# Optimization experiments

Measured on AMD Instinct MI355X. Metric: run time of the kernel, lower is better.

Reference implementation:

```python
import jax, jax.numpy as jnp
import numpy as np

# --- problem constants (match init_kwargs / input_specs) ---
FS = 50.0            # sampling rate (Hz)
WINDOW_FREQ = 0.5    # running-abs-mean window (Hz); >0 -> RAM whitening branch
F1, F2 = 0.1, 10.0   # taper corner frequencies (Hz)
NCH, NPTS = 1000, 30000
XCOR = 2 * NPTS - 1          # 59999
FAST = 65536                 # nextpow2(XCOR)


def setup_inputs() -> dict:
    key = jax.random.key(0)
    k1, k2 = jax.random.split(key)
    return {
        "data1": jax.random.normal(k1, (NCH, NPTS), dtype=jnp.float32),
        "data2": jax.random.normal(k2, (NCH, NPTS), dtype=jnp.float32),
    }


def _running_abs_mean_whiten(rfft, nwin):
    """Vectorized equivalent of per-channel running_absolute_mean:
    pad |spec| by nwin edge values each side, box-filter (scipy 'same'
    alignment => window tmp[i+off+1 : i+off+1+nwin], off=(nwin-1)//2),
    then divide spectrum by the smoothed magnitude."""
    nch, nf = rfft.shape
    off = (nwin - 1) // 2
    a = jnp.abs(rfft)  # [nch, nf]
    tmp = jnp.concatenate(
        [jnp.broadcast_to(a[:, :1], (nch, nwin)), a,
         jnp.broadcast_to(a[:, -1:], (nch, nwin))], axis=1)  # [nch, nf+2*nwin]
    cs = jnp.pad(jnp.cumsum(tmp, axis=1), ((0, 0), (1, 0)))   # leading zero
    smoothed = (cs[:, off + 1 + nwin: off + 1 + nwin + nf]
                - cs[:, off + 1: off + 1 + nf]) / nwin
    return jnp.nan_to_num(rfft / smoothed)


def _spectral_whitening(rfft, df):
    nf = rfft.shape[-1]
    idxf1 = int(np.floor(F1 / df))
    idxf2 = int(np.ceil(F2 / df))
    nwin = int(WINDOW_FREQ / df)
    w = _running_abs_mean_whiten(rfft, nwin)
    # cosine-squared tapers outside [f1, f2]
    taper_lo = jnp.cos(jnp.linspace(np.pi / 2, np.pi, idxf1)) ** 2
    taper_hi = jnp.cos(jnp.linspace(np.pi, np.pi / 2, nf - idxf2)) ** 2
    w = w.at[:, :idxf1].multiply(taper_lo)
    w = w.at[:, idxf2:].multiply(taper_hi)
    return w


def reference(data1, data2):
    df = FS / FAST
    f1 = jnp.fft.rfft(data1, n=FAST, axis=-1)
    f2 = jnp.fft.rfft(data2, n=FAST, axis=-1)
    f1 = _spectral_whitening(f1, df)
    f2 = _spectral_whitening(f2, df)
    cc = jnp.fft.irfft(jnp.conj(f1) * f2, n=FAST, axis=-1)  # [nch, FAST]
    cc = jnp.roll(cc, FAST // 2, axis=-1)
    start = FAST // 2 - XCOR // 2
    return cc[:, start:start + XCOR]  # [nch, 2*npts-1]
```

## Files before the change

### kernel.cpp

```cpp
#include <hip/hip_runtime.h>

#define PI_F 3.14159265358979323846f

#define NCH   1000
#define NPTS  30000
#define NHALF 15000
#define NFFT  32768
#define NBF32 1024
#define STR   32770
#define XCOR  59999

#define UC 0.99518472667219693f
#define US 0.09801714032956060f

__device__ __forceinline__ float2 cadd(float2 a, float2 b){ return make_float2(a.x+b.x, a.y+b.y); }
__device__ __forceinline__ float2 csub(float2 a, float2 b){ return make_float2(a.x-b.x, a.y-b.y); }
__device__ __forceinline__ float2 cmul(float2 a, float2 b){ return make_float2(a.x*b.x - a.y*b.y, a.x*b.y + a.y*b.x); }
__device__ __forceinline__ float2 conjmul(float2 a, float2 b){
  return make_float2(a.x*b.x + a.y*b.y, a.x*b.y - a.y*b.x);
}

template<int S>
__device__ __forceinline__ float2 mulIs(float2 z){ return make_float2(-(float)S*z.y, (float)S*z.x); }

template<int S>
__device__ __forceinline__ void dft8(float2 v[8]){
  const float r2 = 0.7071067811865476f;
  const float sf = (float)S;
  float2 ea=cadd(v[0],v[4]), eb=csub(v[0],v[4]);
  float2 ec=cadd(v[2],v[6]), ed=csub(v[2],v[6]);
  float2 oa=cadd(v[1],v[5]), ob=csub(v[1],v[5]);
  float2 oc=cadd(v[3],v[7]), od=csub(v[3],v[7]);
  float2 ied=mulIs<S>(ed), iod=mulIs<S>(od);
  float2 E0=cadd(ea,ec), E2=csub(ea,ec), E1=cadd(eb,ied), E3=csub(eb,ied);
  float2 O0=cadd(oa,oc), O2=csub(oa,oc), O1=cadd(ob,iod), O3=csub(ob,iod);
  float2 T1 = make_float2(r2*(O1.x - sf*O1.y), r2*(O1.y + sf*O1.x));
  float2 T2 = mulIs<S>(O2);
  float2 T3 = make_float2(r2*(-O3.x - sf*O3.y), r2*(sf*O3.x - O3.y));
  v[0]=cadd(E0,O0); v[4]=csub(E0,O0);
  v[1]=cadd(E1,T1); v[5]=csub(E1,T1);
  v[2]=cadd(E2,T2); v[6]=csub(E2,T2);
  v[3]=cadd(E3,T3); v[7]=csub(E3,T3);
}

template<int S>
__device__ __forceinline__ void dft4(float2 v[4]){
  float2 t0=cadd(v[0],v[2]), t1=csub(v[0],v[2]);
  float2 t2=cadd(v[1],v[3]), t3=mulIs<S>(csub(v[1],v[3]));
  v[0]=cadd(t0,t2); v[2]=csub(t0,t2);
  v[1]=cadd(t1,t3); v[3]=csub(t1,t3);
}

template<int S>
__device__ __forceinline__ void dft32(float2 v[32]){
  constexpr float TC[22] = {
    1.f, 0.98078528040323044f, 0.92387953251128674f, 0.83146961230254524f,
    0.70710678118654757f, 0.55557023301960218f, 0.38268343236508978f, 0.19509032201612825f,
    0.f, -0.19509032201612825f, -0.38268343236508978f, -0.55557023301960218f,
    -0.70710678118654757f, -0.83146961230254524f, -0.92387953251128674f, -0.98078528040323044f,
    -1.f, -0.98078528040323044f, -0.92387953251128674f, -0.83146961230254524f,
    -0.70710678118654757f, -0.55557023301960218f };
  constexpr float TS[22] = {
    0.f, 0.19509032201612825f, 0.38268343236508978f, 0.55557023301960218f,
    0.70710678118654757f, 0.83146961230254524f, 0.92387953251128674f, 0.98078528040323044f,
    1.f, 0.98078528040323044f, 0.92387953251128674f, 0.83146961230254524f,
    0.70710678118654757f, 0.55557023301960218f, 0.38268343236508978f, 0.19509032201612825f,
    0.f, -0.19509032201612825f, -0.38268343236508978f, -0.55557023301960218f,
    -0.70710678118654757f, -0.83146961230254524f };
  float2 y[4][8];
  #pragma unroll
  for (int b = 0; b < 4; ++b)
    #pragma unroll
    for (int a = 0; a < 8; ++a) y[b][a] = v[4*a + b];
  #pragma unroll
  for (int b = 0; b < 4; ++b) dft8<S>(y[b]);
  #pragma unroll
  for (int b = 1; b < 4; ++b)
    #pragma unroll
    for (int k1 = 1; k1 < 8; ++k1) {
      int m = b*k1;
      float2 w = make_float2(TC[m], (float)S * TS[m]);
      y[b][k1] = cmul(y[b][k1], w);
    }
  #pragma unroll
  for (int k1 = 0; k1 < 8; ++k1) {
    float2 z[4] = { y[0][k1], y[1][k1], y[2][k1], y[3][k1] };
    dft4<S>(z);
    #pragma unroll
    for (int k2 = 0; k2 < 4; ++k2) v[k1 + 8*k2] = z[k2];
  }
}

template<int S>
__device__ __forceinline__ void stage_twiddle32(float2 v[32], float ang){
  float s1,c1,s8,c8;
  __sincosf(ang, &s1, &c1);
  __sincosf(8.f*ang, &s8, &c8);
  float2 w1 = make_float2(c1, s1), w8 = make_float2(c8, s8);
  float2 w16 = cmul(w8, w8), w24 = cmul(w16, w8);
  float2 base[4] = { make_float2(1.f, 0.f), w8, w16, w24 };
  #pragma unroll
  for (int m = 0; m < 4; ++m) {
    float2 wr = base[m];
    if (m > 0) v[8*m] = cmul(v[8*m], wr);
    #pragma unroll
    for (int l = 1; l < 8; ++l) { wr = cmul(wr, w1); v[8*m+l] = cmul(v[8*m+l], wr); }
  }
}

__global__ __launch_bounds__(256) void fft_fwd_fused(const float* __restrict__ d1, const float* __restrict__ d2,
                                                     float2* __restrict__ out, int cb, int ch0)
{
  __shared__ float2 lds[256*33];
  const int bid = blockIdx.x;
  const int c = bid >> 2, b = bid & 3;
  const int t = threadIdx.x;
  const float* src = (c < cb) ? (d1 + (size_t)(ch0 + c) * NPTS)
                              : (d2 + (size_t)(ch0 + c - cb) * NPTS);
  const float2* src2 = reinterpret_cast<const float2*>(src);

  const int j1 = 8*b + (t & 7) + 32*(t >> 3);
  float2 v[32];
  #pragma unroll
  for (int r = 0; r < 32; ++r) {
    int m = j1 + (r << 10);
    v[r] = (m < NHALF) ? src2[m] : make_float2(0.f, 0.f);
  }
  dft32<-1>(v);
  #pragma unroll
  for (int r = 0; r < 32; ++r) lds[t*33 + r] = v[r];
  __syncthreads();

  const int d = t >> 5, jm = t & 31;
  #pragma unroll
  for (int r = 0; r < 32; ++r) v[r] = lds[(d + 8*r)*33 + jm];
  stage_twiddle32<-1>(v, -(2.0f*PI_F) * (float)jm * (1.0f/1024.0f));
  dft32<-1>(v);
  const int j2 = 256*b + t;
  float2* dst = out + (size_t)c * STR + ((j2 >> 5) << 10) + jm;
  #pragma unroll
  for (int r = 0; r < 32; ++r) dst[(size_t)(r << 5)] = v[r];
}

template<int LG, int S>
__global__ __launch_bounds__(256) void fft_pass32(const float2* __restrict__ in, float2* __restrict__ out)
{
  int tid = blockIdx.x*256 + threadIdx.x;
  int c = tid >> 10;
  int j = tid & (NBF32-1);
  const float2* src = in + (size_t)c * STR;
  float2 v[32];
  #pragma unroll
  for (int r = 0; r < 32; ++r) v[r] = src[j + (r << 10)];
  constexpr int NS = 1 << LG;
  int jm = j & (NS - 1);
  if constexpr (LG > 0) {
    float ang = (float)S * (2.0f*PI_F) * (float)jm / (float)(NS*32);
    stage_twiddle32<S>(v, ang);
  }
  dft32<S>(v);
  int idxD = ((j >> LG) << (LG+5)) + jm;
  float2* dst = out + (size_t)c * STR + idxD;
  #pragma unroll
  for (int r = 0; r < 32; ++r) dst[(size_t)(r << LG)] = v[r];
}

__device__ __forceinline__ int padidx(int m){ return m + (m >> 5); }

__global__ __launch_bounds__(1024) void whiten_kernel(float2* __restrict__ buf)
{
  const int ch = blockIdx.x;
  const int t  = threadIdx.x;
  float2* Z = buf + (size_t)ch * STR;
  __shared__ float s[33793];
  __shared__ float wsums[16];

  float2 X[33];
  #pragma unroll
  for (int i = 0; i < 33; ++i) {
    int k = i*1024 + t;
    if (i < 32 || t == 0) {
      float2 zk = Z[k & (NFFT-1)];
      float2 zn = Z[(NFFT - k) & (NFFT-1)];
      float2 xe = make_float2(0.5f*(zk.x+zn.x), 0.5f*(zk.y-zn.y));
      float2 xh = make_float2(0.5f*(zk.x-zn.x), 0.5f*(zk.y+zn.y));
      float2 xo = make_float2(xh.y, -xh.x);
      float ang = -PI_F * (float)k * (1.0f/32768.0f);
      float sn, cs; __sincosf(ang, &sn, &cs);
      float2 w = make_float2(cs, sn);
      X[i] = cadd(xe, cmul(w, xo));
      s[padidx(k)] = sqrtf(X[i].x*X[i].x + X[i].y*X[i].y);
    }
  }
  __syncthreads();

  const int base = t*32;
  float sum = 0.f;
  #pragma unroll
  for (int q = 0; q < 32; ++q) sum += s[padidx(base+q)];
  if (t == 1023) sum += s[padidx(32768)];
  const int lane = t & 63, wid = t >> 6;
  float v = sum;
  #pragma unroll
  for (int off = 1; off < 64; off <<= 1) {
    float u = __shfl_up(v, off);
    if (lane >= off) v += u;
  }
  if (lane == 63) wsums[wid] = v;
  __syncthreads();
  float wexcl = 0.f;
  for (int w = 0; w < 16; ++w) wexcl += (w < wid) ? wsums[w] : 0.f;
  float run = wexcl + (v - sum);
  #pragma unroll
  for (int q = 0; q < 32; ++q) {
    int idx = padidx(base+q);
    run += s[idx];
    s[idx] = run;
  }
  if (t == 1023) { int idx = padidx(32768); run += s[idx]; s[idx] = run; }
  __syncthreads();

  const float a0 = s[padidx(0)];
  const float alast = s[padidx(32768)] - s[padidx(32767)];
  #pragma unroll
  for (int i = 0; i < 33; ++i) {
    int k = i*1024 + t;
    if (i < 32 || t == 0) {
      int hi = k + 327; if (hi > 32768) hi = 32768;
      int lom1 = k - 328;
      float Shi = s[padidx(hi)];
      float Slo = (lom1 >= 0) ? s[padidx(lom1)] : 0.f;
      float lc = (k < 327) ? (float)(327 - k) : 0.f;
      float rc = (k > 32441) ? (float)(k - 32441) : 0.f;
      float smoothed = (lc*a0 + (Shi - Slo) + rc*alast) * (1.0f/655.0f);
      float2 wv;
      if (smoothed > 0.f) {
        float inv = 1.0f / smoothed;
        wv = make_float2(X[i].x*inv, X[i].y*inv);
      } else wv = make_float2(0.f, 0.f);
      float tp = 1.0f;
      if (k < 131)        { float th = (float)k * (PI_F/260.0f);           float sn = __sinf(th); tp = sn*sn; }
      else if (k >= 13108){ float th = (float)(k-13108) * (PI_F/39320.0f); float cs = __cosf(th); tp = cs*cs; }
      wv.x *= tp; wv.y *= tp;
      Z[k] = wv;
    }
  }
}

__device__ __forceinline__ float2 pack_zinv(float2 Ck, float2 Cm, float2 pw){
  const float scale = 1.0f/32768.0f;
  float2 xe = make_float2(0.5f*(Ck.x+Cm.x), 0.5f*(Ck.y-Cm.y));
  float2 d  = make_float2(0.5f*(Ck.x-Cm.x), 0.5f*(Ck.y+Cm.y));
  float2 xo = cmul(pw, d);
  return make_float2((xe.x - xo.y)*scale, (xe.y + xo.x)*scale);
}

__global__ __launch_bounds__(256) void cross_inv0_pair(const float2* __restrict__ W,
                                                       float2* __restrict__ out0, int cb)
{
  __shared__ float2 zbs[256*33];
  const int bid = blockIdx.x;
  const int c = bid >> 1;
  const int t = threadIdx.x;
  const int p = ((bid & 1) << 8) + t;
  const float2* W1 = W + (size_t)c * STR;
  const float2* W2 = W + (size_t)(cb + c) * STR;
  const float scale = 1.0f/32768.0f;
  float2 zA[32];
  float2* zB = zbs + t*33;

  if (p != 0) {
    const int q = 1024 - p;
    float sp, cp; __sincosf(PI_F*(float)p*(1.0f/32768.0f), &sp, &cp);
    float2 pw = make_float2(cp, sp);
    const float2 pstep = make_float2(UC, US);
    #pragma unroll
    for (int r = 0; r < 32; ++r) {
      int m  = p + (r << 10);
      int mm = q + ((31 - r) << 10);
      float2 Ck = conjmul(W1[m],  W2[m]);
      float2 Cm = conjmul(W1[mm], W2[mm]);
      zA[r]    = pack_zinv(Ck, Cm, pw);
      zB[31-r] = pack_zinv(Cm, Ck, make_float2(-pw.x, pw.y));
      pw = cmul(pw, pstep);
    }
  } else {
    {
      float2 Ck = conjmul(W1[0], W2[0]);
      float2 Cm = conjmul(W1[32768], W2[32768]);
      zA[0] = pack_zinv(Ck, Cm, make_float2(1.f, 0.f));
    }
    #pragma unroll
    for (int i = 1; i < 16; ++i) {
      int k = i << 10, km = 32768 - k;
      float2 Ck = conjmul(W1[k],  W2[k]);
      float2 Cm = conjmul(W1[km], W2[km]);
      float sp2, cp2; __sincosf(PI_F*(float)k*(1.0f/32768.0f), &sp2, &cp2);
      zA[i]    = pack_zinv(Ck, Cm, make_float2(cp2, sp2));
      zA[32-i] = pack_zinv(Cm, Ck, make_float2(-cp2, sp2));
    }
    {
      float2 Ck = conjmul(W1[16384], W2[16384]);
      zA[16] = make_float2(Ck.x*scale, -Ck.y*scale);
    }
    #pragma unroll
    for (int i = 0; i < 16; ++i) {
      int k = (i << 10) + 512, km = 32768 - k;
      float2 Ck = conjmul(W1[k],  W2[k]);
      float2 Cm = conjmul(W1[km], W2[km]);
      float sp2, cp2; __sincosf(PI_F*(float)k*(1.0f/32768.0f), &sp2, &cp2);
      zB[i]    = pack_zinv(Ck, Cm, make_float2(cp2, sp2));
      zB[31-i] = pack_zinv(Cm, Ck, make_float2(-cp2, sp2));
    }
  }

  dft32<1>(zA);
  {
    float4* o4 = reinterpret_cast<float4*>(out0 + (size_t)c*STR + (size_t)p*32);
    #pragma unroll
    for (int r = 0; r < 32; r += 2)
      o4[r>>1] = make_float4(zA[r].x, zA[r].y, zA[r+1].x, zA[r+1].y);
  }
  {
    float2 zq[32];
    #pragma unroll
    for (int r = 0; r < 32; ++r) zq[r] = zB[r];
    dft32<1>(zq);
    const int jout = (p == 0) ? 512 : (1024 - p);
    float4* o4 = reinterpret_cast<float4*>(out0 + (size_t)c*STR + (size_t)jout*32);
    #pragma unroll
    for (int r = 0; r < 32; r += 2)
      o4[r>>1] = make_float4(zq[r].x, zq[r].y, zq[r+1].x, zq[r+1].y);
  }
}

__global__ __launch_bounds__(256) void fft_inv_fused2(const float2* __restrict__ in,
                                                      float* __restrict__ out, int ch0)
{
  __shared__ float2 lds[32*268];
  const int c = blockIdx.x;
  const int b = blockIdx.y;
  const int t = threadIdx.x;
  const int li = t & 7, s = t >> 3;
  const int l = 8*b + li;
  const float2* src = in + (size_t)c * STR;

  {
    const int j1 = l + 32*s;
    float2 v[32];
    #pragma unroll
    for (int r = 0; r < 32; ++r) v[r] = src[j1 + (r << 10)];
    stage_twiddle32<1>(v, (2.0f*PI_F) * (float)l * (1.0f/1024.0f));
    dft32<1>(v);
    #pragma unroll
    for (int r = 0; r < 32; ++r) lds[s*268 + li*33 + r] = v[r];
  }
  __syncthreads();

  const int q = s;
  const int j2 = l + 32*q;
  float2 v[32];
  #pragma unroll
  for (int r2 = 0; r2 < 32; ++r2) v[r2] = lds[r2*268 + li*33 + q];
  stage_twiddle32<1>(v, (2.0f*PI_F) * (float)j2 * (1.0f/32768.0f));
  dft32<1>(v);

  float* o = out + (size_t)(ch0 + c) * XCOR;
  #pragma unroll
  for (int r = 0; r < 32; ++r) {
    int n = j2 + (r << 10);
    int m = 2*n;
    int j1o = (m <= 29999) ? (m + 29999) : ((m >= 35537) ? (m - 35537) : -1);
    if (j1o >= 0) o[j1o] = v[r].x;
    int m2 = m + 1;
    int j2o = (m2 <= 29999) ? (m2 + 29999) : ((m2 >= 35537) ? (m2 - 35537) : -1);
    if (j2o >= 0) o[j2o] = v[r].y;
  }
}

__global__ void diag_kernel(float* out, float vv){ if (threadIdx.x==0 && blockIdx.x==0) out[0] = vv; }

extern "C" void kernel_launch(void* const* d_in, const int* in_sizes, int n_in,
                              void* d_out, int out_size, void* d_ws, size_t ws_size,
                              hipStream_t stream)
{
  const float* d1 = (const float*)d_in[0];
  const float* d2 = (const float*)d_in[1];
  float* out = (float*)d_out;

  const size_t bytesPerCh = 2ULL * 2ULL * (size_t)STR * sizeof(float2);
  int CB = (int)(ws_size / bytesPerCh);
  if (CB > NCH) CB = NCH;
  if (CB < 1) { diag_kernel<<<1,1,0,stream>>>(out, (float)ws_size); return; }

  float2* bufA = (float2*)d_ws;
  float2* bufB = bufA + (size_t)2 * CB * STR;

  for (int ch0 = 0; ch0 < NCH; ch0 += CB) {
    int cb = (NCH - ch0 < CB) ? (NCH - ch0) : CB;
    int nch2 = 2*cb;
    dim3 thr(256);

    fft_fwd_fused     <<<dim3(nch2*4), thr, 0, stream>>>(d1, d2, bufA, cb, ch0);
    fft_pass32<10,-1> <<<dim3(nch2*4), thr, 0, stream>>>(bufA, bufB);

    whiten_kernel     <<<dim3(nch2), dim3(1024), 0, stream>>>(bufB);

    cross_inv0_pair   <<<dim3(cb*2), thr, 0, stream>>>(bufB, bufA, cb);

    fft_inv_fused2    <<<dim3(cb, 4), thr, 0, stream>>>(bufA, out, ch0);
  }
}
```

Measured before the change: 1.298 ms.

## Split fused inverse FFT into two passes and use recurrence twiddles in whitening

The whitening kernel now computes its unpack twiddles and cosine taper values with complex-multiply recurrences instead of a sincos call per element, which cuts transcendental work. The fused two-stage inverse FFT kernel, which exchanged data through shared memory, is replaced by a separate fft_pass32 launch followed by a simpler final radix-32 kernel. That adds a global-memory round trip and an extra launch but removes the LDS transpose and its barrier. The recurrences can accumulate float rounding error over 33 steps.

```diff
diff --git a/kernel.cpp b/kernel.cpp
--- a/kernel.cpp
+++ b/kernel.cpp
@@ -176,20 +176,23 @@
   __shared__ float wsums[16];
 
   float2 X[33];
-  #pragma unroll
-  for (int i = 0; i < 33; ++i) {
-    int k = i*1024 + t;
-    if (i < 32 || t == 0) {
-      float2 zk = Z[k & (NFFT-1)];
-      float2 zn = Z[(NFFT - k) & (NFFT-1)];
-      float2 xe = make_float2(0.5f*(zk.x+zn.x), 0.5f*(zk.y-zn.y));
-      float2 xh = make_float2(0.5f*(zk.x-zn.x), 0.5f*(zk.y+zn.y));
-      float2 xo = make_float2(xh.y, -xh.x);
-      float ang = -PI_F * (float)k * (1.0f/32768.0f);
-      float sn, cs; __sincosf(ang, &sn, &cs);
-      float2 w = make_float2(cs, sn);
-      X[i] = cadd(xe, cmul(w, xo));
-      s[padidx(k)] = sqrtf(X[i].x*X[i].x + X[i].y*X[i].y);
+  {
+    float s0, c0; __sincosf(-PI_F*(float)t*(1.0f/32768.0f), &s0, &c0);
+    float2 uw = make_float2(c0, s0);
+    const float2 uwstep = make_float2(UC, -US);
+    #pragma unroll
+    for (int i = 0; i < 33; ++i) {
+      int k = i*1024 + t;
+      if (i < 32 || t == 0) {
+        float2 zk = Z[k & (NFFT-1)];
+        float2 zn = Z[(NFFT - k) & (NFFT-1)];
+        float2 xe = make_float2(0.5f*(zk.x+zn.x), 0.5f*(zk.y-zn.y));
+        float2 xh = make_float2(0.5f*(zk.x-zn.x), 0.5f*(zk.y+zn.y));
+        float2 xo = make_float2(xh.y, -xh.x);
+        X[i] = cadd(xe, cmul(uw, xo));
+        s[padidx(k)] = sqrtf(X[i].x*X[i].x + X[i].y*X[i].y);
+      }
+      uw = cmul(uw, uwstep);
     }
   }
   __syncthreads();
@@ -222,27 +225,34 @@
 
   const float a0 = s[padidx(0)];
   const float alast = s[padidx(32768)] - s[padidx(32767)];
-  #pragma unroll
-  for (int i = 0; i < 33; ++i) {
-    int k = i*1024 + t;
-    if (i < 32 || t == 0) {
-      int hi = k + 327; if (hi > 32768) hi = 32768;
-      int lom1 = k - 328;
-      float Shi = s[padidx(hi)];
-      float Slo = (lom1 >= 0) ? s[padidx(lom1)] : 0.f;
-      float lc = (k < 327) ? (float)(327 - k) : 0.f;
-      float rc = (k > 32441) ? (float)(k - 32441) : 0.f;
-      float smoothed = (lc*a0 + (Shi - Slo) + rc*alast) * (1.0f/655.0f);
-      float2 wv;
-      if (smoothed > 0.f) {
-        float inv = 1.0f / smoothed;
-        wv = make_float2(X[i].x*inv, X[i].y*inv);
-      } else wv = make_float2(0.f, 0.f);
-      float tp = 1.0f;
-      if (k < 131)        { float th = (float)k * (PI_F/260.0f);           float sn = __sinf(th); tp = sn*sn; }
-      else if (k >= 13108){ float th = (float)(k-13108) * (PI_F/39320.0f); float cs = __cosf(th); tp = cs*cs; }
-      wv.x *= tp; wv.y *= tp;
-      Z[k] = wv;
+  {
+    float su, cu; __sincosf(((float)t - 13108.0f)*(PI_F/39320.0f), &su, &cu);
+    float2 tu = make_float2(cu, su);
+    float tss, tcc; __sincosf(1024.0f*(PI_F/39320.0f), &tss, &tcc);
+    const float2 tustep = make_float2(tcc, tss);
+    #pragma unroll
+    for (int i = 0; i < 33; ++i) {
+      int k = i*1024 + t;
+      if (i < 32 || t == 0) {
+        int hi = k + 327; if (hi > 32768) hi = 32768;
+        int lom1 = k - 328;
+        float Shi = s[padidx(hi)];
+        float Slo = (lom1 >= 0) ? s[padidx(lom1)] : 0.f;
+        float lc = (k < 327) ? (float)(327 - k) : 0.f;
+        float rc = (k > 32441) ? (float)(k - 32441) : 0.f;
+        float smoothed = (lc*a0 + (Shi - Slo) + rc*alast) * (1.0f/655.0f);
+        float2 wv;
+        if (smoothed > 0.f) {
+          float inv = 1.0f / smoothed;
+          wv = make_float2(X[i].x*inv, X[i].y*inv);
+        } else wv = make_float2(0.f, 0.f);
+        float tp = 1.0f;
+        if (k < 131)        { float sn = __sinf((float)k * (PI_F/260.0f)); tp = sn*sn; }
+        else if (k >= 13108) tp = tu.x*tu.x;
+        wv.x *= tp; wv.y *= tp;
+        Z[k] = wv;
+      }
+      tu = cmul(tu, tustep);
     }
   }
 }
@@ -334,47 +344,28 @@
   }
 }
 
-__global__ __launch_bounds__(256) void fft_inv_fused2(const float2* __restrict__ in,
-                                                      float* __restrict__ out, int ch0)
-{
-  __shared__ float2 lds[32*268];
-  const int c = blockIdx.x;
-  const int b = blockIdx.y;
-  const int t = threadIdx.x;
-  const int li = t & 7, s = t >> 3;
-  const int l = 8*b + li;
+__global__ __launch_bounds__(256) void fft_inv_final32(const float2* __restrict__ in, float* __restrict__ out, int ch0)
+{
+  int tid = blockIdx.x*256 + threadIdx.x;
+  int c = tid >> 10;
+  int j = tid & (NBF32-1);
   const float2* src = in + (size_t)c * STR;
-
-  {
-    const int j1 = l + 32*s;
-    float2 v[32];
-    #pragma unroll
-    for (int r = 0; r < 32; ++r) v[r] = src[j1 + (r << 10)];
-    stage_twiddle32<1>(v, (2.0f*PI_F) * (float)l * (1.0f/1024.0f));
-    dft32<1>(v);
-    #pragma unroll
-    for (int r = 0; r < 32; ++r) lds[s*268 + li*33 + r] = v[r];
-  }
-  __syncthreads();
-
-  const int q = s;
-  const int j2 = l + 32*q;
   float2 v[32];
   #pragma unroll
-  for (int r2 = 0; r2 < 32; ++r2) v[r2] = lds[r2*268 + li*33 + q];
-  stage_twiddle32<1>(v, (2.0f*PI_F) * (float)j2 * (1.0f/32768.0f));
+  for (int r = 0; r < 32; ++r) v[r] = src[j + (r << 10)];
+  float ang = (2.0f*PI_F) * (float)j * (1.0f/32768.0f);
+  stage_twiddle32<1>(v, ang);
   dft32<1>(v);
-
   float* o = out + (size_t)(ch0 + c) * XCOR;
   #pragma unroll
   for (int r = 0; r < 32; ++r) {
-    int n = j2 + (r << 10);
+    int n = j + (r << 10);
     int m = 2*n;
-    int j1o = (m <= 29999) ? (m + 29999) : ((m >= 35537) ? (m - 35537) : -1);
-    if (j1o >= 0) o[j1o] = v[r].x;
+    int j1 = (m <= 29999) ? (m + 29999) : ((m >= 35537) ? (m - 35537) : -1);
+    if (j1 >= 0) o[j1] = v[r].x;
     int m2 = m + 1;
-    int j2o = (m2 <= 29999) ? (m2 + 29999) : ((m2 >= 35537) ? (m2 - 35537) : -1);
-    if (j2o >= 0) o[j2o] = v[r].y;
+    int j2 = (m2 <= 29999) ? (m2 + 29999) : ((m2 >= 35537) ? (m2 - 35537) : -1);
+    if (j2 >= 0) o[j2] = v[r].y;
   }
 }
 
@@ -408,6 +399,7 @@
 
     cross_inv0_pair   <<<dim3(cb*2), thr, 0, stream>>>(bufB, bufA, cb);
 
-    fft_inv_fused2    <<<dim3(cb, 4), thr, 0, stream>>>(bufA, out, ch0);
-  }
-}
+    fft_pass32<5,1>   <<<dim3(cb*4), thr, 0, stream>>>(bufA, bufB);
+    fft_inv_final32   <<<dim3(cb*4), thr, 0, stream>>>(bufB, out, ch0);
+  }
+}
```

Result: faster. 1.180 ms, median of 2 (-9.1%).
